# Kernel tuning notes

Measured on AMD Instinct MI355X. Metric: run time of the kernel, lower is better.

The kernel has to match this reference:

```python
import jax, jax.numpy as jnp
import numpy as np

D = 512      # input_dim
A = 512      # inner_att_dim
H = 8        # outer_att_head_n
DK = 64      # outer_att_dim
HS = 4       # outer_score_att_head_n
DKS = 64     # outer_score_att_dim
FF = 2048    # ffn_dim
P = 512      # past_edit_n
E = 256      # number of edit groups
NM = 4       # n_modes
NEG = -999999.0
EPS = 1e-5


def layer_norm(x, w, b):
    mu = x.mean(-1, keepdims=True)
    var = ((x - mu) ** 2).mean(-1, keepdims=True)
    return (x - mu) / jnp.sqrt(var + EPS) * w + b


def setup_inputs() -> dict:
    rng = np.random.default_rng(0)
    lens = rng.integers(128, 385, size=E)
    N = int(lens.sum())
    key = jax.random.key(0)
    ks = jax.random.split(key, 24)

    def w(k, shape, s=0.02):
        return jax.random.normal(k, shape, jnp.float32) * s

    return {
        "x": w(ks[0], (N, D), 1.0),
        "past_rep": w(ks[1], (1, P, D), 1.0),
        "edit_lens": jnp.asarray(lens, jnp.int32),
        "mode": jax.random.randint(ks[2], (N,), 0, NM),
        # inner attention trans1 / trans2
        "t1w1": w(ks[3], (D, A)), "t1b1": jnp.zeros((A,), jnp.float32),
        "t1w2": w(ks[4], (A, D)), "t1b2": jnp.zeros((D,), jnp.float32),
        "t2w1": w(ks[5], (D, A)), "t2b1": jnp.zeros((A,), jnp.float32),
        "t2w2": w(ks[6], (A, 1)), "t2b2": jnp.zeros((1,), jnp.float32),
        # outer attention (with values)
        "oq_w": w(ks[7], (D, H * DK)), "oq_b": jnp.zeros((H * DK,), jnp.float32),
        "ok_w": w(ks[8], (D, H * DK)), "ok_b": jnp.zeros((H * DK,), jnp.float32),
        "ov_w": w(ks[9], (D, H * DK)), "ov_b": jnp.zeros((H * DK,), jnp.float32),
        "oo_w": w(ks[10], (H * DK, D)), "oo_b": jnp.zeros((D,), jnp.float32),
        # outer score attention (scores only)
        "sq_w": w(ks[11], (D, HS * DKS)), "sq_b": jnp.zeros((HS * DKS,), jnp.float32),
        "sk_w": w(ks[12], (D, HS * DKS)), "sk_b": jnp.zeros((HS * DKS,), jnp.float32),
        # feedforward
        "f1w": w(ks[13], (D, FF)), "f1b": jnp.zeros((FF,), jnp.float32),
        "f2w": w(ks[14], (FF, D)), "f2b": jnp.zeros((D,), jnp.float32),
        # layer norms
        "ln1w": jnp.ones((D,), jnp.float32), "ln1b": jnp.zeros((D,), jnp.float32),
        "ln2w": jnp.ones((D,), jnp.float32), "ln2b": jnp.zeros((D,), jnp.float32),
        "ln3w": jnp.ones((D,), jnp.float32), "ln3b": jnp.zeros((D,), jnp.float32),
        # FiLM mode tables (torch init: scale=1, shift=0)
        "mscale": jnp.ones((NM, D), jnp.float32),
        "mshift": jnp.zeros((NM, D), jnp.float32),
    }


def reference(x, past_rep, edit_lens, mode,
              t1w1, t1b1, t1w2, t1b2, t2w1, t2b1, t2w2, t2b2,
              oq_w, oq_b, ok_w, ok_b, ov_w, ov_b, oo_w, oo_b,
              sq_w, sq_b, sk_w, sk_b,
              f1w, f1b, f2w, f2b,
              ln1w, ln1b, ln2w, ln2b, ln3w, ln3b,
              mscale, mshift):
    N = x.shape[0]
    Eg = edit_lens.shape[0]
    Pn = past_rep.shape[1]
    # token -> edit-group id (replaces split/pad/mask gather with segment ops)
    seg = jnp.repeat(jnp.arange(Eg), edit_lens, total_repeat_length=N)

    # ---- inner attention (segment softmax) ----
    att_x = jnp.maximum(x @ t1w1 + t1b1, 0) @ t1w2 + t1b2          # [N, D]
    s = (jnp.maximum(att_x @ t2w1 + t2b1, 0) @ t2w2 + t2b2)[:, 0]  # [N]
    smax = jax.lax.stop_gradient(jax.ops.segment_max(s, seg, num_segments=Eg))
    p = jnp.exp(s - smax[seg])
    den = jax.ops.segment_sum(p, seg, num_segments=Eg)
    wgt = p / den[seg]
    weighted = att_x * wgt[:, None]                                # == masked padded att_x*att_s
    sample_rep = jax.ops.segment_sum(weighted, seg, num_segments=Eg)  # [E, D]
    x = layer_norm(x + weighted, ln1w, ln1b)

    sr = sample_rep[None]                                          # [1, E, D]
    new_rep = jnp.concatenate([past_rep, sr], axis=1)              # [1, P+E, D]
    mask = jnp.triu(jnp.ones((Eg, Pn + Eg), x.dtype), k=Pn + 1) * NEG

    # ---- outer attention (multi-head, with values) ----
    q = (sr @ oq_w + oq_b).reshape(1, Eg, H, DK)
    k = (new_rep @ ok_w + ok_b).reshape(1, Pn + Eg, H, DK)
    v = (new_rep @ ov_w + ov_b).reshape(1, Pn + Eg, H, DK)
    sc = jnp.einsum('bqhd,bkhd->bhqk', q, k) / jnp.sqrt(jnp.asarray(DK, x.dtype)) + mask
    a = jax.nn.softmax(sc, axis=-1)
    o = jnp.einsum('bhqk,bkhd->bqhd', a, v).reshape(1, Eg, H * DK) @ oo_w + oo_b
    x = layer_norm(x + o[0][seg], ln2w, ln2b)                      # repeat_interleave via gather

    # ---- outer score attention (scores only, head-mean) ----
    q2 = (sr @ sq_w + sq_b).reshape(1, Eg, HS, DKS)
    k2 = (new_rep @ sk_w + sk_b).reshape(1, Pn + Eg, HS, DKS)
    sc2 = jnp.einsum('bqhd,bkhd->bhqk', q2, k2) / jnp.sqrt(jnp.asarray(DKS, x.dtype)) + mask
    a2 = jax.nn.softmax(sc2, axis=-1).mean(1)[0]                   # [E, P+E]
    u = jnp.diagonal(a2, offset=Pn)                                # [E]
    pflip = jnp.flip(jnp.cumprod(jnp.flip(1.0 - u)))               # reversed cumprod
    update_scale = jnp.concatenate([u[:-1] * pflip[1:], u[-1:]])
    past_update_scale = pflip[0]

    # ---- FFN + FiLM gate ----
    ffn = jnp.maximum(x @ f1w + f1b, 0) @ f2w + f2b
    x = layer_norm(x + ffn, ln3w, ln3b)
    pre = x * mscale[mode] + mshift[mode]
    x = jnp.maximum(pre, 0) + x
    return (x, past_update_scale, update_scale, new_rep)
```

## Files before the change

kernel.cpp:

```cpp
#include <hip/hip_runtime.h>
#include <hip/hip_bf16.h>
#include <cmath>


#define DD 512
#define FF 2048
#define PP 512
#define NEG_BIG (-1e30f)
#define LDT 68
#define LBUF (128 * 32)

typedef __attribute__((ext_vector_type(8))) short shortx8;
typedef __attribute__((ext_vector_type(4))) float floatx4;

__device__ __forceinline__ unsigned short f2b(float f) {
    unsigned int u = __float_as_uint(f);
    unsigned int r = (u + 0x7fffu + ((u >> 16) & 1u)) >> 16;
    return (unsigned short)r;
}
__device__ __forceinline__ float b2f(unsigned short h) {
    return __uint_as_float(((unsigned int)h) << 16);
}

__device__ __forceinline__ void async_copy16(const void* g, void* l) {
    __builtin_amdgcn_global_load_lds(
        (const __attribute__((address_space(1))) unsigned int*)g,
        (__attribute__((address_space(3))) unsigned int*)l, 16, 0, 0);
}

__device__ __forceinline__ float wave_sum64(float v) {
#pragma unroll
    for (int d = 32; d > 0; d >>= 1) v += __shfl_xor(v, d, 64);
    return v;
}

template<int OUT_BF16, int RELU>
__global__ __launch_bounds__(256) void gemm_bf16_kernel(
    const unsigned short* __restrict__ A, const unsigned short* __restrict__ Bt,
    const float* __restrict__ bias, void* __restrict__ C,
    int M, int N, int K)
{
    __shared__ unsigned short As[3][LBUF];
    __shared__ unsigned short Bs[3][LBUF];

    int t = threadIdx.x;
    int w = t >> 6, l = t & 63;

    int nwg = gridDim.x * gridDim.y;
    int bid = blockIdx.x + blockIdx.y * gridDim.x;
    int qch = nwg >> 3, rch = nwg & 7;
    int xcd = bid & 7, lo = bid >> 3;
    int swz = (xcd < rch ? xcd * (qch + 1) : rch * (qch + 1) + (xcd - rch) * qch) + lo;
    int bm = (swz / gridDim.y) * 128;
    int bn = (swz % gridDim.y) * 128;

    int wm = (w >> 1) * 64, wn = (w & 1) * 64;

    floatx4 acc[4][4];
#pragma unroll
    for (int i = 0; i < 4; ++i)
#pragma unroll
        for (int j = 0; j < 4; ++j)
#pragma unroll
            for (int r = 0; r < 4; ++r) acc[i][j][r] = 0.f;

    int s0 = t, s1 = 256 + t;
    int ar0 = s0 >> 2, ar1 = s1 >> 2;
    int ak0 = ((s0 & 3) ^ ((ar0 >> 1) & 3)) * 8;
    int ak1 = ((s1 & 3) ^ ((ar1 >> 1) & 3)) * 8;
    int am0 = min(bm + ar0, M - 1);
    int am1 = min(bm + ar1, M - 1);
    const unsigned short* Ap0 = A + (size_t)am0 * K + ak0;
    const unsigned short* Ap1 = A + (size_t)am1 * K + ak1;
    const unsigned short* Bp0 = Bt + (size_t)(bn + ar0) * K + ak0;
    const unsigned short* Bp1 = Bt + (size_t)(bn + ar1) * K + ak1;

    int o0 = (w * 64) * 8, o1 = (256 + w * 64) * 8;

    int fr = l & 15, fq = l >> 4;
    int sw = (fr >> 1) & 3;
    int aoff = (wm + fr) * 32 + ((fq ^ sw) * 8);
    int boff = (wn + fr) * 32 + ((fq ^ sw) * 8);

    int nt = K >> 5;

    async_copy16(Ap0, &As[0][o0]);
    async_copy16(Ap1, &As[0][o1]);
    async_copy16(Bp0, &Bs[0][o0]);
    async_copy16(Bp1, &Bs[0][o1]);
    async_copy16(Ap0 + 32, &As[1][o0]);
    async_copy16(Ap1 + 32, &As[1][o1]);
    async_copy16(Bp0 + 32, &Bs[1][o0]);
    async_copy16(Bp1 + 32, &Bs[1][o1]);
    asm volatile("s_waitcnt vmcnt(4)" ::: "memory");
    __builtin_amdgcn_s_barrier();
    asm volatile("" ::: "memory");

    int b0 = 0, b1 = 1, b2 = 2;
    for (int tt = 0; tt < nt; ++tt) {
        if (tt + 2 < nt) {
            int k2 = (tt + 2) << 5;
            unsigned short* Ad = &As[0][0] + b2 * LBUF;
            unsigned short* Bd = &Bs[0][0] + b2 * LBUF;
            async_copy16(Ap0 + k2, Ad + o0);
            async_copy16(Ap1 + k2, Ad + o1);
            async_copy16(Bp0 + k2, Bd + o0);
            async_copy16(Bp1 + k2, Bd + o1);
        }
        {
            const unsigned short* Ab = &As[0][0] + b0 * LBUF;
            const unsigned short* Bb = &Bs[0][0] + b0 * LBUF;
            shortx8 af[4], bf[4];
#pragma unroll
            for (int i = 0; i < 4; ++i) af[i] = *(const shortx8*)&Ab[aoff + i * 16 * 32];
#pragma unroll
            for (int j = 0; j < 4; ++j) bf[j] = *(const shortx8*)&Bb[boff + j * 16 * 32];
#pragma unroll
            for (int i = 0; i < 4; ++i)
#pragma unroll
                for (int j = 0; j < 4; ++j)
                    acc[i][j] = __builtin_amdgcn_mfma_f32_16x16x32_bf16(bf[j], af[i], acc[i][j], 0, 0, 0);
        }
        if (tt + 2 < nt) {
            asm volatile("s_waitcnt vmcnt(4)" ::: "memory");
        } else {
            asm volatile("s_waitcnt vmcnt(0)" ::: "memory");
        }
        __builtin_amdgcn_s_barrier();
        asm volatile("" ::: "memory");
        int tmp = b0; b0 = b1; b1 = b2; b2 = tmp;
    }

    float4 bb[4];
#pragma unroll
    for (int j = 0; j < 4; ++j)
        bb[j] = *(const float4*)&bias[bn + wn + j * 16 + fq * 4];

#pragma unroll
    for (int i = 0; i < 4; ++i) {
        int row = bm + wm + i * 16 + fr;
        if (row >= M) continue;
#pragma unroll
        for (int j = 0; j < 4; ++j) {
            int col = bn + wn + j * 16 + fq * 4;
            float v0 = acc[i][j][0] + bb[j].x;
            float v1 = acc[i][j][1] + bb[j].y;
            float v2 = acc[i][j][2] + bb[j].z;
            float v3 = acc[i][j][3] + bb[j].w;
            if (RELU) {
                v0 = fmaxf(v0, 0.f); v1 = fmaxf(v1, 0.f);
                v2 = fmaxf(v2, 0.f); v3 = fmaxf(v3, 0.f);
            }
            if (OUT_BF16) {
                ushort4 o;
                o.x = f2b(v0); o.y = f2b(v1); o.z = f2b(v2); o.w = f2b(v3);
                *(ushort4*)&((unsigned short*)C)[(size_t)row * N + col] = o;
            } else {
                float4 o;
                o.x = v0; o.y = v1; o.z = v2; o.w = v3;
                *(float4*)&((float*)C)[(size_t)row * N + col] = o;
            }
        }
    }
}

__global__ void cvt_b16_kernel(const float* __restrict__ in, unsigned short* __restrict__ out, size_t n4)
{
    size_t i = (size_t)blockIdx.x * blockDim.x + threadIdx.x;
    if (i >= n4) return;
    float4 v = ((const float4*)in)[i];
    ushort4 o;
    o.x = f2b(v.x); o.y = f2b(v.y); o.z = f2b(v.z); o.w = f2b(v.w);
    ((ushort4*)out)[i] = o;
}

__global__ __launch_bounds__(256) void transpose_b16_kernel(
    const float* __restrict__ W, unsigned short* __restrict__ Wt, int Kd, int Nd)
{
    __shared__ float tile[32][33];
    int bx = blockIdx.x * 32;
    int by = blockIdx.y * 32;
    int tx = threadIdx.x & 31, ty = threadIdx.x >> 5;
#pragma unroll
    for (int i = 0; i < 32; i += 8)
        tile[ty + i][tx] = W[(size_t)(by + ty + i) * Nd + bx + tx];
    __syncthreads();
#pragma unroll
    for (int i = 0; i < 32; i += 8)
        Wt[(size_t)(bx + ty + i) * Kd + by + tx] = f2b(tile[tx][ty + i]);
}

__global__ void bcat_kernel(const float* __restrict__ okb, const float* __restrict__ ovb,
                            const float* __restrict__ oqb, const float* __restrict__ skb,
                            const float* __restrict__ sqb, float* __restrict__ bcat)
{
    int i = blockIdx.x * 256 + threadIdx.x;
    float v;
    if      (i < 512)  v = okb[i];
    else if (i < 1024) v = ovb[i - 512];
    else if (i < 1536) v = oqb[i - 1024];
    else if (i < 1792) v = skb[i - 1536];
    else               v = sqb[i - 1792];
    bcat[i] = v;
}

__global__ __launch_bounds__(256) void gemm_kernel(
    const float* __restrict__ A, const float* __restrict__ W,
    const float* __restrict__ bias, float* __restrict__ C,
    int M, int N, int K, int relu)
{
    __shared__ float As[16][68];
    __shared__ float Ws[16][68];
    int t  = threadIdx.x;
    int tx = t & 15, ty = t >> 4;
    int bm = blockIdx.x * 64, bn = blockIdx.y * 64;
    float acc[4][4] = {};

    for (int k0 = 0; k0 < K; k0 += 16) {
#pragma unroll
        for (int e = 0; e < 4; ++e) {
            int idx = t + e * 256;
            int kk = idx & 15, m = idx >> 4;
            int row = bm + m;
            As[kk][m] = (row < M) ? A[(size_t)row * K + k0 + kk] : 0.f;
        }
#pragma unroll
        for (int e = 0; e < 4; ++e) {
            int idx = t + e * 256;
            int n = idx & 63, kk = idx >> 6;
            Ws[kk][n] = W[(size_t)(k0 + kk) * N + bn + n];
        }
        __syncthreads();
#pragma unroll
        for (int kk = 0; kk < 16; ++kk) {
            float4 a4 = *(const float4*)&As[kk][ty * 4];
            float4 b4 = *(const float4*)&Ws[kk][tx * 4];
            float av[4] = {a4.x, a4.y, a4.z, a4.w};
            float bv[4] = {b4.x, b4.y, b4.z, b4.w};
#pragma unroll
            for (int i = 0; i < 4; ++i)
#pragma unroll
                for (int j = 0; j < 4; ++j)
                    acc[i][j] += av[i] * bv[j];
        }
        __syncthreads();
    }

#pragma unroll
    for (int i = 0; i < 4; ++i) {
        int row = bm + ty * 4 + i;
        if (row >= M) continue;
        int col = bn + tx * 4;
        float4 bb = *(const float4*)&bias[col];
        float4 r;
        r.x = acc[i][0] + bb.x; r.y = acc[i][1] + bb.y;
        r.z = acc[i][2] + bb.z; r.w = acc[i][3] + bb.w;
        if (relu) {
            r.x = fmaxf(r.x, 0.f); r.y = fmaxf(r.y, 0.f);
            r.z = fmaxf(r.z, 0.f); r.w = fmaxf(r.w, 0.f);
        }
        *(float4*)&C[(size_t)row * N + col] = r;
    }
}

__global__ __launch_bounds__(64) void rowdot512_b16_kernel(
    const unsigned short* __restrict__ A, const float* __restrict__ w,
    const float* __restrict__ bptr, float* __restrict__ out)
{
    int row = blockIdx.x;
    int lane = threadIdx.x;
    int col = lane * 8;
    shortx8 a8 = *(const shortx8*)(A + (size_t)row * DD + col);
    float4 w0 = *(const float4*)(w + col);
    float4 w1 = *(const float4*)(w + col + 4);
    float v = b2f((unsigned short)a8[0]) * w0.x + b2f((unsigned short)a8[1]) * w0.y
            + b2f((unsigned short)a8[2]) * w0.z + b2f((unsigned short)a8[3]) * w0.w
            + b2f((unsigned short)a8[4]) * w1.x + b2f((unsigned short)a8[5]) * w1.y
            + b2f((unsigned short)a8[6]) * w1.z + b2f((unsigned short)a8[7]) * w1.w;
#pragma unroll
    for (int d = 32; d > 0; d >>= 1) v += __shfl_down(v, d, 64);
    if (lane == 0) out[row] = v + bptr[0];
}

__global__ void seg_offsets_kernel(const int* __restrict__ lens, int* __restrict__ offs, int E)
{
    if (threadIdx.x == 0 && blockIdx.x == 0) {
        int acc = 0;
        for (int g = 0; g < E; ++g) { offs[g] = acc; acc += lens[g]; }
        offs[E] = acc;
    }
}

__global__ void fill_seg_kernel(const int* __restrict__ offs, int* __restrict__ seg)
{
    int g = blockIdx.x;
    int o = offs[g], e = offs[g + 1];
    for (int i = o + threadIdx.x; i < e; i += blockDim.x) seg[i] = g;
}

__global__ __launch_bounds__(384) void seg_softmax_kernel(
    const float* __restrict__ s, const int* __restrict__ offs, float* __restrict__ wgt)
{
    __shared__ float red[8];
    int g = blockIdx.x;
    int o = offs[g], len = offs[g + 1] - o;
    int t = threadIdx.x;
    int lane = t & 63, wid = t >> 6;

    float v = (t < len) ? s[o + t] : NEG_BIG;
    float m = v;
#pragma unroll
    for (int d = 32; d > 0; d >>= 1) m = fmaxf(m, __shfl_down(m, d, 64));
    if (lane == 0) red[wid] = m;
    __syncthreads();
    if (t == 0) {
        float mm = red[0];
        for (int i = 1; i < 6; ++i) mm = fmaxf(mm, red[i]);
        red[6] = mm;
    }
    __syncthreads();
    float M = red[6];

    float p = (t < len) ? expf(v - M) : 0.f;
    float sum = p;
#pragma unroll
    for (int d = 32; d > 0; d >>= 1) sum += __shfl_down(sum, d, 64);
    if (lane == 0) red[wid] = sum;
    __syncthreads();
    if (t == 0) {
        float ss = red[0];
        for (int i = 1; i < 6; ++i) ss += red[i];
        red[7] = ss;
    }
    __syncthreads();
    if (t < len) wgt[o + t] = p / red[7];
}

__global__ __launch_bounds__(256) void seg_wsum_part_kernel(
    const unsigned short* __restrict__ att_x, const float* __restrict__ wgt,
    const int* __restrict__ offs, float* __restrict__ part)
{
    __shared__ float sm[4][DD];
    int g = blockIdx.x, ch = blockIdx.y;
    int o = offs[g], e = offs[g + 1];
    int len = e - o;
    int per = (len + 7) >> 3;
    int s = o + ch * per;
    int en = min(s + per, e);

    int t = threadIdx.x, lane = t & 63, w = t >> 6;
    int col = lane * 8;
    float acc[8] = {};
    for (int i = s + w; i < en; i += 4) {
        float wt = wgt[i];
        shortx8 v = *(const shortx8*)(att_x + (size_t)i * DD + col);
#pragma unroll
        for (int j = 0; j < 8; ++j)
            acc[j] += b2f((unsigned short)v[j]) * wt;
    }
#pragma unroll
    for (int j = 0; j < 8; ++j) sm[w][col + j] = acc[j];
    __syncthreads();

    float* pr = part + ((size_t)g * 8 + ch) * DD;
#pragma unroll
    for (int j = 0; j < 2; ++j) {
        int c = t * 2 + j;
        pr[c] = (sm[0][c] + sm[1][c]) + (sm[2][c] + sm[3][c]);
    }
}

__global__ __launch_bounds__(256) void seg_wsum_reduce_kernel(
    const float* __restrict__ part, float* __restrict__ rep)
{
    int g = blockIdx.x;
    int t = threadIdx.x;
#pragma unroll
    for (int j = 0; j < 2; ++j) {
        int c = t * 2 + j;
        float s = 0.f;
#pragma unroll
        for (int ch = 0; ch < 8; ++ch)
            s += part[((size_t)g * 8 + ch) * DD + c];
        rep[(size_t)g * DD + c] = s;
    }
}

__global__ __launch_bounds__(256) void ln1_kernel(
    const float* __restrict__ x, const unsigned short* __restrict__ att_x,
    const float* __restrict__ wgt, const float* __restrict__ w,
    const float* __restrict__ b, float* __restrict__ out, int N)
{
    int row = blockIdx.x * 4 + (threadIdx.x >> 6);
    if (row >= N) return;
    int col = (threadIdx.x & 63) * 8;
    const float* xr = x + (size_t)row * DD + col;
    const unsigned short* ar = att_x + (size_t)row * DD + col;
    float wr = wgt[row];
    float4 x0 = *(const float4*)xr;
    float4 x1 = *(const float4*)(xr + 4);
    shortx8 a8 = *(const shortx8*)ar;
    float v[8];
    v[0] = x0.x + b2f((unsigned short)a8[0]) * wr;
    v[1] = x0.y + b2f((unsigned short)a8[1]) * wr;
    v[2] = x0.z + b2f((unsigned short)a8[2]) * wr;
    v[3] = x0.w + b2f((unsigned short)a8[3]) * wr;
    v[4] = x1.x + b2f((unsigned short)a8[4]) * wr;
    v[5] = x1.y + b2f((unsigned short)a8[5]) * wr;
    v[6] = x1.z + b2f((unsigned short)a8[6]) * wr;
    v[7] = x1.w + b2f((unsigned short)a8[7]) * wr;
    float s = (v[0] + v[1] + v[2] + v[3]) + (v[4] + v[5] + v[6] + v[7]);
    float mean = wave_sum64(s) * (1.f / 512.f);
    float q = 0.f;
#pragma unroll
    for (int j = 0; j < 8; ++j) { v[j] -= mean; q += v[j] * v[j]; }
    float rstd = rsqrtf(wave_sum64(q) * (1.f / 512.f) + 1e-5f);
    float4 w0 = *(const float4*)(w + col), w1 = *(const float4*)(w + col + 4);
    float4 b0 = *(const float4*)(b + col), b1 = *(const float4*)(b + col + 4);
    float4 o0, o1;
    o0.x = v[0] * rstd * w0.x + b0.x; o0.y = v[1] * rstd * w0.y + b0.y;
    o0.z = v[2] * rstd * w0.z + b0.z; o0.w = v[3] * rstd * w0.w + b0.w;
    o1.x = v[4] * rstd * w1.x + b1.x; o1.y = v[5] * rstd * w1.y + b1.y;
    o1.z = v[6] * rstd * w1.z + b1.z; o1.w = v[7] * rstd * w1.w + b1.w;
    *(float4*)(out + (size_t)row * DD + col) = o0;
    *(float4*)(out + (size_t)row * DD + col + 4) = o1;
}

__global__ __launch_bounds__(256) void ln2_kernel(
    float* __restrict__ xb, const float* __restrict__ o,
    const int* __restrict__ seg, const float* __restrict__ w,
    const float* __restrict__ b, unsigned short* __restrict__ xb16, int N)
{
    int row = blockIdx.x * 4 + (threadIdx.x >> 6);
    if (row >= N) return;
    int col = (threadIdx.x & 63) * 8;
    int g = seg[row];
    const float* xr = xb + (size_t)row * DD + col;
    const float* orow = o + (size_t)g * DD + col;
    float4 x0 = *(const float4*)xr;
    float4 x1 = *(const float4*)(xr + 4);
    float4 a0 = *(const float4*)orow;
    float4 a1 = *(const float4*)(orow + 4);
    float v[8];
    v[0] = x0.x + a0.x; v[1] = x0.y + a0.y; v[2] = x0.z + a0.z; v[3] = x0.w + a0.w;
    v[4] = x1.x + a1.x; v[5] = x1.y + a1.y; v[6] = x1.z + a1.z; v[7] = x1.w + a1.w;
    float s = (v[0] + v[1] + v[2] + v[3]) + (v[4] + v[5] + v[6] + v[7]);
    float mean = wave_sum64(s) * (1.f / 512.f);
    float q = 0.f;
#pragma unroll
    for (int j = 0; j < 8; ++j) { v[j] -= mean; q += v[j] * v[j]; }
    float rstd = rsqrtf(wave_sum64(q) * (1.f / 512.f) + 1e-5f);
    float4 w0 = *(const float4*)(w + col), w1 = *(const float4*)(w + col + 4);
    float4 b0 = *(const float4*)(b + col), b1 = *(const float4*)(b + col + 4);
    float y[8];
    y[0] = v[0] * rstd * w0.x + b0.x; y[1] = v[1] * rstd * w0.y + b0.y;
    y[2] = v[2] * rstd * w0.z + b0.z; y[3] = v[3] * rstd * w0.w + b0.w;
    y[4] = v[4] * rstd * w1.x + b1.x; y[5] = v[5] * rstd * w1.y + b1.y;
    y[6] = v[6] * rstd * w1.z + b1.z; y[7] = v[7] * rstd * w1.w + b1.w;
    float4 o0, o1;
    o0.x = y[0]; o0.y = y[1]; o0.z = y[2]; o0.w = y[3];
    o1.x = y[4]; o1.y = y[5]; o1.z = y[6]; o1.w = y[7];
    *(float4*)(xb + (size_t)row * DD + col) = o0;
    *(float4*)(xb + (size_t)row * DD + col + 4) = o1;
    ushort4 h0, h1;
    h0.x = f2b(y[0]); h0.y = f2b(y[1]); h0.z = f2b(y[2]); h0.w = f2b(y[3]);
    h1.x = f2b(y[4]); h1.y = f2b(y[5]); h1.z = f2b(y[6]); h1.w = f2b(y[7]);
    *(ushort4*)(xb16 + (size_t)row * DD + col) = h0;
    *(ushort4*)(xb16 + (size_t)row * DD + col + 4) = h1;
}

__global__ __launch_bounds__(256) void ln3_film_kernel(
    const float* __restrict__ xb, const unsigned short* __restrict__ ffn,
    const int* __restrict__ mode, const float* __restrict__ w,
    const float* __restrict__ b, const float* __restrict__ msc,
    const float* __restrict__ msh, float* __restrict__ out, int N)
{
    int row = blockIdx.x * 4 + (threadIdx.x >> 6);
    if (row >= N) return;
    int col = (threadIdx.x & 63) * 8;
    int md = mode[row];
    const float* xr = xb + (size_t)row * DD + col;
    const unsigned short* fr = ffn + (size_t)row * DD + col;
    float4 x0 = *(const float4*)xr;
    float4 x1 = *(const float4*)(xr + 4);
    shortx8 f8 = *(const shortx8*)fr;
    float v[8];
    v[0] = x0.x + b2f((unsigned short)f8[0]);
    v[1] = x0.y + b2f((unsigned short)f8[1]);
    v[2] = x0.z + b2f((unsigned short)f8[2]);
    v[3] = x0.w + b2f((unsigned short)f8[3]);
    v[4] = x1.x + b2f((unsigned short)f8[4]);
    v[5] = x1.y + b2f((unsigned short)f8[5]);
    v[6] = x1.z + b2f((unsigned short)f8[6]);
    v[7] = x1.w + b2f((unsigned short)f8[7]);
    float s = (v[0] + v[1] + v[2] + v[3]) + (v[4] + v[5] + v[6] + v[7]);
    float mean = wave_sum64(s) * (1.f / 512.f);
    float q = 0.f;
#pragma unroll
    for (int j = 0; j < 8; ++j) { v[j] -= mean; q += v[j] * v[j]; }
    float rstd = rsqrtf(wave_sum64(q) * (1.f / 512.f) + 1e-5f);
    float4 w0 = *(const float4*)(w + col), w1 = *(const float4*)(w + col + 4);
    float4 b0 = *(const float4*)(b + col), b1 = *(const float4*)(b + col + 4);
    const float* mscr = msc + (size_t)md * DD + col;
    const float* mshr = msh + (size_t)md * DD + col;
    float4 s0 = *(const float4*)mscr, s1 = *(const float4*)(mscr + 4);
    float4 t0 = *(const float4*)mshr, t1 = *(const float4*)(mshr + 4);
    float y[8], sc[8], sh[8], wv[8], bv[8];
    wv[0] = w0.x; wv[1] = w0.y; wv[2] = w0.z; wv[3] = w0.w;
    wv[4] = w1.x; wv[5] = w1.y; wv[6] = w1.z; wv[7] = w1.w;
    bv[0] = b0.x; bv[1] = b0.y; bv[2] = b0.z; bv[3] = b0.w;
    bv[4] = b1.x; bv[5] = b1.y; bv[6] = b1.z; bv[7] = b1.w;
    sc[0] = s0.x; sc[1] = s0.y; sc[2] = s0.z; sc[3] = s0.w;
    sc[4] = s1.x; sc[5] = s1.y; sc[6] = s1.z; sc[7] = s1.w;
    sh[0] = t0.x; sh[1] = t0.y; sh[2] = t0.z; sh[3] = t0.w;
    sh[4] = t1.x; sh[5] = t1.y; sh[6] = t1.z; sh[7] = t1.w;
    float r[8];
#pragma unroll
    for (int j = 0; j < 8; ++j) {
        y[j] = v[j] * rstd * wv[j] + bv[j];
        float p = y[j] * sc[j] + sh[j];
        r[j] = fmaxf(p, 0.f) + y[j];
    }
    float4 o0, o1;
    o0.x = r[0]; o0.y = r[1]; o0.z = r[2]; o0.w = r[3];
    o1.x = r[4]; o1.y = r[5]; o1.z = r[6]; o1.w = r[7];
    *(float4*)(out + (size_t)row * DD + col) = o0;
    *(float4*)(out + (size_t)row * DD + col + 4) = o1;
}

__global__ void newrep_kernel(const float* __restrict__ past, const float* __restrict__ rep,
                              float* __restrict__ out, int total)
{
    int i = blockIdx.x * blockDim.x + threadIdx.x;
    if (i >= total) return;
    out[i] = (i < PP * DD) ? past[i] : rep[i - PP * DD];
}

__global__ __launch_bounds__(256) void attn_scores_kernel(
    const float* __restrict__ proj, float* __restrict__ S, int pe)
{
    int q0 = blockIdx.x * 64;
    int k0 = blockIdx.y * 64;
    int h  = blockIdx.z;
    if (k0 > PP + q0 + 63) return;

    int qcol = (h < 8) ? (1024 + h * 64) : (1792 + (h - 8) * 64);
    int kcol = (h < 8) ? (h * 64)        : (1536 + (h - 8) * 64);

    __shared__ float Qs[64][LDT];
    __shared__ float Ks[64][LDT];
    int t = threadIdx.x;
    int r = t >> 2, c4 = (t & 3) * 16;
    const float* qsrc = proj + (size_t)(PP + q0 + r) * 2048 + qcol + c4;
    const float* ksrc = proj + (size_t)(k0 + r) * 2048 + kcol + c4;
#pragma unroll
    for (int e = 0; e < 4; ++e) {
        float4 v = *(const float4*)(qsrc + e * 4);
        Qs[c4 + e * 4 + 0][r] = v.x; Qs[c4 + e * 4 + 1][r] = v.y;
        Qs[c4 + e * 4 + 2][r] = v.z; Qs[c4 + e * 4 + 3][r] = v.w;
        float4 u = *(const float4*)(ksrc + e * 4);
        Ks[c4 + e * 4 + 0][r] = u.x; Ks[c4 + e * 4 + 1][r] = u.y;
        Ks[c4 + e * 4 + 2][r] = u.z; Ks[c4 + e * 4 + 3][r] = u.w;
    }
    __syncthreads();

    int tx = t & 15, ty = t >> 4;
    float acc[4][4] = {};
#pragma unroll 4
    for (int d = 0; d < 64; ++d) {
        float4 a = *(const float4*)&Qs[d][ty * 4];
        float4 b = *(const float4*)&Ks[d][tx * 4];
        float av[4] = {a.x, a.y, a.z, a.w};
        float bv[4] = {b.x, b.y, b.z, b.w};
#pragma unroll
        for (int i = 0; i < 4; ++i)
#pragma unroll
            for (int j = 0; j < 4; ++j)
                acc[i][j] += av[i] * bv[j];
    }

    float* Sh = S + ((size_t)h * 256 + q0) * pe + k0;
#pragma unroll
    for (int i = 0; i < 4; ++i) {
        float4 o;
        o.x = acc[i][0] * 0.125f; o.y = acc[i][1] * 0.125f;
        o.z = acc[i][2] * 0.125f; o.w = acc[i][3] * 0.125f;
        *(float4*)&Sh[(size_t)(ty * 4 + i) * pe + tx * 4] = o;
    }
}

__global__ __launch_bounds__(256) void attn_softmax_kernel(
    float* __restrict__ S, float* __restrict__ u4, int pe)
{
    __shared__ float red[8];
    int q = blockIdx.x;
    int h = blockIdx.y;
    int limq = PP + q;
    float* row = S + ((size_t)h * 256 + q) * pe;
    int t = threadIdx.x;
    int lane = t & 63, wid = t >> 6;

    float m = NEG_BIG;
    for (int k = t; k <= limq; k += 256) m = fmaxf(m, row[k]);
#pragma unroll
    for (int d = 32; d > 0; d >>= 1) m = fmaxf(m, __shfl_xor(m, d, 64));
    if (lane == 0) red[wid] = m;
    __syncthreads();
    float M = fmaxf(fmaxf(red[0], red[1]), fmaxf(red[2], red[3]));

    float s = 0.f;
    for (int k = t; k <= limq; k += 256) s += expf(row[k] - M);
#pragma unroll
    for (int d = 32; d > 0; d >>= 1) s += __shfl_xor(s, d, 64);
    if (lane == 0) red[4 + wid] = s;
    __syncthreads();
    float SUM = (red[4] + red[5]) + (red[6] + red[7]);
    float inv = 1.f / SUM;

    if (h < 8) {
        for (int k = t; k < pe; k += 256)
            row[k] = (k <= limq) ? expf(row[k] - M) * inv : 0.f;
    } else {
        if (t == 0) u4[q * 4 + (h - 8)] = expf(row[limq] - M) * inv;
    }
}

__global__ __launch_bounds__(256) void attn_pv_kernel(
    const float* __restrict__ S, const float* __restrict__ proj,
    float* __restrict__ ob, int pe)
{
    __shared__ float Ps[64][36];
    __shared__ float Vs[64][LDT];
    int q0 = blockIdx.x * 32;
    int h  = blockIdx.y;
    int ktiles = (PP + q0 + 31) / 64 + 1;

    int t = threadIdx.x;
    int tx = t & 15, ty = t >> 4;
    int rp = t >> 3, c8 = (t & 7) * 8;
    int rv = t >> 2, c16 = (t & 3) * 16;
    float acc[2][4] = {};

    for (int kt = 0; kt < ktiles; ++kt) {
        int k0 = kt * 64;
        const float* psrc = S + ((size_t)h * 256 + q0 + rp) * pe + k0 + c8;
        const float* vsrc = proj + (size_t)(k0 + rv) * 2048 + 512 + h * 64 + c16;
#pragma unroll
        for (int e = 0; e < 2; ++e) {
            float4 v = *(const float4*)(psrc + e * 4);
            Ps[c8 + e * 4 + 0][rp] = v.x; Ps[c8 + e * 4 + 1][rp] = v.y;
            Ps[c8 + e * 4 + 2][rp] = v.z; Ps[c8 + e * 4 + 3][rp] = v.w;
        }
#pragma unroll
        for (int e = 0; e < 4; ++e)
            *(float4*)&Vs[rv][c16 + e * 4] = *(const float4*)(vsrc + e * 4);
        __syncthreads();

#pragma unroll 8
        for (int kk = 0; kk < 64; ++kk) {
            float2 a = *(const float2*)&Ps[kk][ty * 2];
            float4 b = *(const float4*)&Vs[kk][tx * 4];
            float av[2] = {a.x, a.y};
            float bv[4] = {b.x, b.y, b.z, b.w};
#pragma unroll
            for (int i = 0; i < 2; ++i)
#pragma unroll
                for (int j = 0; j < 4; ++j)
                    acc[i][j] += av[i] * bv[j];
        }
        __syncthreads();
    }

#pragma unroll
    for (int i = 0; i < 2; ++i) {
        float4 o;
        o.x = acc[i][0]; o.y = acc[i][1]; o.z = acc[i][2]; o.w = acc[i][3];
        *(float4*)&ob[(size_t)(q0 + ty * 2 + i) * DD + h * 64 + tx * 4] = o;
    }
}

__global__ void finalize_kernel(const float* __restrict__ u4, float* __restrict__ out_past,
                                float* __restrict__ out_us, int E)
{
    if (threadIdx.x == 0 && blockIdx.x == 0) {
        float uE = 0.25f * (u4[(E - 1) * 4] + u4[(E - 1) * 4 + 1] + u4[(E - 1) * 4 + 2] + u4[(E - 1) * 4 + 3]);
        out_us[E - 1] = uE;
        float pf = 1.f;
        for (int i = E - 1; i >= 0; --i) {
            float u = 0.25f * (u4[i * 4] + u4[i * 4 + 1] + u4[i * 4 + 2] + u4[i * 4 + 3]);
            if (i < E - 1) out_us[i] = u * pf;
            pf = (1.f - u) * pf;
        }
        out_past[0] = pf;
    }
}

extern "C" void kernel_launch(void* const* d_in, const int* in_sizes, int n_in,
                              void* d_out, int out_size, void* d_ws, size_t ws_size,
                              hipStream_t stream)
{
    const float* x    = (const float*)d_in[0];
    const float* past = (const float*)d_in[1];
    const int*   lens = (const int*)d_in[2];
    const int*   mode = (const int*)d_in[3];
    const float* t1w1 = (const float*)d_in[4];
    const float* t1b1 = (const float*)d_in[5];
    const float* t1w2 = (const float*)d_in[6];
    const float* t1b2 = (const float*)d_in[7];
    const float* t2w1 = (const float*)d_in[8];
    const float* t2b1 = (const float*)d_in[9];
    const float* t2w2 = (const float*)d_in[10];
    const float* t2b2 = (const float*)d_in[11];
    const float* oq_w = (const float*)d_in[12];
    const float* oq_b = (const float*)d_in[13];
    const float* ok_w = (const float*)d_in[14];
    const float* ok_b = (const float*)d_in[15];
    const float* ov_w = (const float*)d_in[16];
    const float* ov_b = (const float*)d_in[17];
    const float* oo_w = (const float*)d_in[18];
    const float* oo_b = (const float*)d_in[19];
    const float* sq_w = (const float*)d_in[20];
    const float* sq_b = (const float*)d_in[21];
    const float* sk_w = (const float*)d_in[22];
    const float* sk_b = (const float*)d_in[23];
    const float* f1w  = (const float*)d_in[24];
    const float* f1b  = (const float*)d_in[25];
    const float* f2w  = (const float*)d_in[26];
    const float* f2b_ = (const float*)d_in[27];
    const float* ln1w = (const float*)d_in[28];
    const float* ln1b = (const float*)d_in[29];
    const float* ln2w = (const float*)d_in[30];
    const float* ln2b = (const float*)d_in[31];
    const float* ln3w = (const float*)d_in[32];
    const float* ln3b = (const float*)d_in[33];
    const float* msc  = (const float*)d_in[34];
    const float* msh  = (const float*)d_in[35];

    int N  = in_sizes[0] / DD;
    int E  = in_sizes[2];
    int PE = PP + E;
    if (N <= 0) return;

    float* out        = (float*)d_out;
    float* out_x      = out;
    float* out_past   = out + (size_t)N * DD;
    float* out_us     = out_past + 1;
    float* out_newrep = out_us + E;

    const int CH = 16384;
    char* wp = (char*)d_ws;
    unsigned short* b16_a = (unsigned short*)wp;  wp += (size_t)N * DD * 2;
    unsigned short* b16_b = (unsigned short*)wp;  wp += (size_t)N * DD * 2;
    unsigned short* ffh   = (unsigned short*)wp;  wp += (size_t)CH * FF * 2;
    unsigned short* wt1   = (unsigned short*)wp;  wp += (size_t)DD * DD * 2;
    unsigned short* wt2   = (unsigned short*)wp;  wp += (size_t)DD * DD * 2;
    unsigned short* wt3   = (unsigned short*)wp;  wp += (size_t)DD * DD * 2;
    unsigned short* wtf1  = (unsigned short*)wp;  wp += (size_t)FF * DD * 2;
    unsigned short* wtf2  = (unsigned short*)wp;  wp += (size_t)DD * FF * 2;
    unsigned short* wtcat = (unsigned short*)wp;  wp += (size_t)2048 * DD * 2;
    unsigned short* nr16  = (unsigned short*)wp;  wp += (size_t)PE * DD * 2;
    float* bcat = (float*)wp;  wp += 2048 * 4;
    float* proj = (float*)wp;  wp += (size_t)PE * 2048 * 4;
    float* sbuf = (float*)wp;  wp += (size_t)N * 4;
    float* wgt  = (float*)wp;  wp += (size_t)N * 4;
    float* rep  = (float*)wp;  wp += (size_t)E * DD * 4;
    float* ob   = (float*)wp;  wp += (size_t)E * DD * 4;
    float* oprj = (float*)wp;  wp += (size_t)E * DD * 4;
    float* u4   = (float*)wp;  wp += (size_t)E * 4 * 4;
    int*   seg  = (int*)wp;    wp += (size_t)N * 4;
    int*   offs = (int*)wp;

    float* part = (float*)ffh;
    float* S    = (float*)ffh;

    int mg128 = (N + 127) / 128;
    int ln_grid = (N + 3) / 4;

    transpose_b16_kernel<<<dim3(DD / 32, DD / 32), 256, 0, stream>>>(t1w1, wt1, DD, DD);
    transpose_b16_kernel<<<dim3(DD / 32, DD / 32), 256, 0, stream>>>(t1w2, wt2, DD, DD);
    transpose_b16_kernel<<<dim3(DD / 32, DD / 32), 256, 0, stream>>>(t2w1, wt3, DD, DD);
    transpose_b16_kernel<<<dim3(FF / 32, DD / 32), 256, 0, stream>>>(f1w, wtf1, DD, FF);
    transpose_b16_kernel<<<dim3(DD / 32, FF / 32), 256, 0, stream>>>(f2w, wtf2, FF, DD);
    transpose_b16_kernel<<<dim3(DD / 32, DD / 32), 256, 0, stream>>>(ok_w, wtcat,              DD, DD);
    transpose_b16_kernel<<<dim3(DD / 32, DD / 32), 256, 0, stream>>>(ov_w, wtcat + 512 * DD,  DD, DD);
    transpose_b16_kernel<<<dim3(DD / 32, DD / 32), 256, 0, stream>>>(oq_w, wtcat + 1024 * DD, DD, DD);
    transpose_b16_kernel<<<dim3(256 / 32, DD / 32), 256, 0, stream>>>(sk_w, wtcat + 1536 * DD, DD, 256);
    transpose_b16_kernel<<<dim3(256 / 32, DD / 32), 256, 0, stream>>>(sq_w, wtcat + 1792 * DD, DD, 256);
    bcat_kernel<<<8, 256, 0, stream>>>(ok_b, ov_b, oq_b, sk_b, sq_b, bcat);

    size_t n4 = (size_t)N * DD / 4;
    cvt_b16_kernel<<<(int)((n4 + 255) / 256), 256, 0, stream>>>(x, b16_a, n4);

    gemm_bf16_kernel<1, 1><<<dim3(mg128, DD / 128), 256, 0, stream>>>(b16_a, wt1, t1b1, b16_b, N, DD, DD);
    gemm_bf16_kernel<1, 0><<<dim3(mg128, DD / 128), 256, 0, stream>>>(b16_b, wt2, t1b2, b16_a, N, DD, DD);
    gemm_bf16_kernel<1, 1><<<dim3(mg128, DD / 128), 256, 0, stream>>>(b16_a, wt3, t2b1, b16_b, N, DD, DD);
    rowdot512_b16_kernel<<<N, 64, 0, stream>>>(b16_b, t2w2, t2b2, sbuf);

    seg_offsets_kernel<<<1, 64, 0, stream>>>(lens, offs, E);
    fill_seg_kernel<<<E, 256, 0, stream>>>(offs, seg);
    seg_softmax_kernel<<<E, 384, 0, stream>>>(sbuf, offs, wgt);
    seg_wsum_part_kernel<<<dim3(E, 8), 256, 0, stream>>>(b16_a, wgt, offs, part);
    seg_wsum_reduce_kernel<<<E, 256, 0, stream>>>(part, rep);
    ln1_kernel<<<ln_grid, 256, 0, stream>>>(x, b16_a, wgt, ln1w, ln1b, out_x, N);

    int nr_total = PE * DD;
    newrep_kernel<<<(nr_total + 255) / 256, 256, 0, stream>>>(past, rep, out_newrep, nr_total);
    cvt_b16_kernel<<<(nr_total / 4 + 255) / 256, 256, 0, stream>>>(out_newrep, nr16, nr_total / 4);

    gemm_bf16_kernel<0, 0><<<dim3(PE / 128, 2048 / 128), 256, 0, stream>>>(nr16, wtcat, bcat, proj, PE, 2048, DD);

    attn_scores_kernel<<<dim3(E / 64, PE / 64, 12), 256, 0, stream>>>(proj, S, PE);
    attn_softmax_kernel<<<dim3(E, 12), 256, 0, stream>>>(S, u4, PE);
    attn_pv_kernel<<<dim3(E / 32, 8), 256, 0, stream>>>(S, proj, ob, PE);
    gemm_kernel<<<dim3(E / 64, DD / 64), 256, 0, stream>>>(ob, oo_w, oo_b, oprj, E, DD, DD, 0);
    ln2_kernel<<<ln_grid, 256, 0, stream>>>(out_x, oprj, seg, ln2w, ln2b, b16_b, N);
    finalize_kernel<<<1, 64, 0, stream>>>(u4, out_past, out_us, E);

    for (int r0 = 0; r0 < N; r0 += CH) {
        int mr = N - r0; if (mr > CH) mr = CH;
        int mgc = (mr + 127) / 128;
        gemm_bf16_kernel<1, 1><<<dim3(mgc, FF / 128), 256, 0, stream>>>(
            b16_b + (size_t)r0 * DD, wtf1, f1b, ffh, mr, FF, DD);
        gemm_bf16_kernel<1, 0><<<dim3(mgc, DD / 128), 256, 0, stream>>>(
            ffh, wtf2, f2b_, b16_a + (size_t)r0 * DD, mr, DD, FF);
    }
    ln3_film_kernel<<<ln_grid, 256, 0, stream>>>(out_x, b16_a, mode, ln3w, ln3b, msc, msh, out_x, N);
}
```

Baseline: 1.412 ms.

## Process two M-tiles per workgroup in bf16 GEMM and enlarge FFN chunk size

Adds a STRIP template parameter so each workgroup computes two consecutive 128-row tiles sharing one continuous pipelined K loop, writing back and resetting accumulators between tiles. The wrapper picks STRIP=2 only when the halved grid still has at least 512 workgroups, cutting workgroup count and launch/prologue overhead. The FFN chunk size now covers all rows when the workspace is large enough, giving fewer, larger GEMM launches. Risks: B tiles are reloaded per strip rather than reused, and fewer workgroups can reduce occupancy balance.

```diff
diff --git a/kernel.cpp b/kernel.cpp
--- a/kernel.cpp
+++ b/kernel.cpp
@@ -34,7 +34,7 @@
     return v;
 }
 
-template<int OUT_BF16, int RELU>
+template<int OUT_BF16, int RELU, int STRIP>
 __global__ __launch_bounds__(256) void gemm_bf16_kernel(
     const unsigned short* __restrict__ A, const unsigned short* __restrict__ Bt,
     const float* __restrict__ bias, void* __restrict__ C,
@@ -51,8 +51,8 @@
     int qch = nwg >> 3, rch = nwg & 7;
     int xcd = bid & 7, lo = bid >> 3;
     int swz = (xcd < rch ? xcd * (qch + 1) : rch * (qch + 1) + (xcd - rch) * qch) + lo;
-    int bm = (swz / gridDim.y) * 128;
-    int bn = (swz % gridDim.y) * 128;
+    int bmb = (swz / gridDim.y) * (128 * STRIP);
+    int bn  = (swz % gridDim.y) * 128;
 
     int wm = (w >> 1) * 64, wn = (w & 1) * 64;
 
@@ -68,10 +68,15 @@
     int ar0 = s0 >> 2, ar1 = s1 >> 2;
     int ak0 = ((s0 & 3) ^ ((ar0 >> 1) & 3)) * 8;
     int ak1 = ((s1 & 3) ^ ((ar1 >> 1) & 3)) * 8;
-    int am0 = min(bm + ar0, M - 1);
-    int am1 = min(bm + ar1, M - 1);
-    const unsigned short* Ap0 = A + (size_t)am0 * K + ak0;
-    const unsigned short* Ap1 = A + (size_t)am1 * K + ak1;
+
+    const unsigned short* Ap0m0 = A + (size_t)min(bmb + ar0, M - 1) * K + ak0;
+    const unsigned short* Ap1m0 = A + (size_t)min(bmb + ar1, M - 1) * K + ak1;
+    const unsigned short* Ap0m1 = Ap0m0;
+    const unsigned short* Ap1m1 = Ap1m0;
+    if (STRIP == 2) {
+        Ap0m1 = A + (size_t)min(bmb + 128 + ar0, M - 1) * K + ak0;
+        Ap1m1 = A + (size_t)min(bmb + 128 + ar1, M - 1) * K + ak1;
+    }
     const unsigned short* Bp0 = Bt + (size_t)(bn + ar0) * K + ak0;
     const unsigned short* Bp1 = Bt + (size_t)(bn + ar1) * K + ak1;
 
@@ -83,29 +88,41 @@
     int boff = (wn + fr) * 32 + ((fq ^ sw) * 8);
 
     int nt = K >> 5;
-
-    async_copy16(Ap0, &As[0][o0]);
-    async_copy16(Ap1, &As[0][o1]);
+    int T  = nt * STRIP;
+
+    async_copy16(Ap0m0, &As[0][o0]);
+    async_copy16(Ap1m0, &As[0][o1]);
     async_copy16(Bp0, &Bs[0][o0]);
     async_copy16(Bp1, &Bs[0][o1]);
-    async_copy16(Ap0 + 32, &As[1][o0]);
-    async_copy16(Ap1 + 32, &As[1][o1]);
+    async_copy16(Ap0m0 + 32, &As[1][o0]);
+    async_copy16(Ap1m0 + 32, &As[1][o1]);
     async_copy16(Bp0 + 32, &Bs[1][o0]);
     async_copy16(Bp1 + 32, &Bs[1][o1]);
     asm volatile("s_waitcnt vmcnt(4)" ::: "memory");
     __builtin_amdgcn_s_barrier();
     asm volatile("" ::: "memory");
 
+    float4 bb[4];
+#pragma unroll
+    for (int j = 0; j < 4; ++j)
+        bb[j] = *(const float4*)&bias[bn + wn + j * 16 + fq * 4];
+
     int b0 = 0, b1 = 1, b2 = 2;
-    for (int tt = 0; tt < nt; ++tt) {
-        if (tt + 2 < nt) {
-            int k2 = (tt + 2) << 5;
+    int ck = 0, cm = 0;
+    for (int tau = 0; tau < T; ++tau) {
+        if (tau + 2 < T) {
+            int t2 = tau + 2;
+            int usem1 = (STRIP == 2 && t2 >= nt) ? 1 : 0;
+            int k2 = t2 - (usem1 ? nt : 0);
+            int kb = k2 << 5;
+            const unsigned short* a0p = usem1 ? Ap0m1 : Ap0m0;
+            const unsigned short* a1p = usem1 ? Ap1m1 : Ap1m0;
             unsigned short* Ad = &As[0][0] + b2 * LBUF;
             unsigned short* Bd = &Bs[0][0] + b2 * LBUF;
-            async_copy16(Ap0 + k2, Ad + o0);
-            async_copy16(Ap1 + k2, Ad + o1);
-            async_copy16(Bp0 + k2, Bd + o0);
-            async_copy16(Bp1 + k2, Bd + o1);
+            async_copy16(a0p + kb, Ad + o0);
+            async_copy16(a1p + kb, Ad + o1);
+            async_copy16(Bp0 + kb, Bd + o0);
+            async_copy16(Bp1 + kb, Bd + o1);
         }
         {
             const unsigned short* Ab = &As[0][0] + b0 * LBUF;
@@ -121,7 +138,7 @@
                 for (int j = 0; j < 4; ++j)
                     acc[i][j] = __builtin_amdgcn_mfma_f32_16x16x32_bf16(bf[j], af[i], acc[i][j], 0, 0, 0);
         }
-        if (tt + 2 < nt) {
+        if (tau + 2 < T) {
             asm volatile("s_waitcnt vmcnt(4)" ::: "memory");
         } else {
             asm volatile("s_waitcnt vmcnt(0)" ::: "memory");
@@ -129,37 +146,46 @@
         __builtin_amdgcn_s_barrier();
         asm volatile("" ::: "memory");
         int tmp = b0; b0 = b1; b1 = b2; b2 = tmp;
-    }
-
-    float4 bb[4];
-#pragma unroll
-    for (int j = 0; j < 4; ++j)
-        bb[j] = *(const float4*)&bias[bn + wn + j * 16 + fq * 4];
-
-#pragma unroll
-    for (int i = 0; i < 4; ++i) {
-        int row = bm + wm + i * 16 + fr;
-        if (row >= M) continue;
-#pragma unroll
-        for (int j = 0; j < 4; ++j) {
-            int col = bn + wn + j * 16 + fq * 4;
-            float v0 = acc[i][j][0] + bb[j].x;
-            float v1 = acc[i][j][1] + bb[j].y;
-            float v2 = acc[i][j][2] + bb[j].z;
-            float v3 = acc[i][j][3] + bb[j].w;
-            if (RELU) {
-                v0 = fmaxf(v0, 0.f); v1 = fmaxf(v1, 0.f);
-                v2 = fmaxf(v2, 0.f); v3 = fmaxf(v3, 0.f);
+
+        if (++ck == nt) {
+            ck = 0;
+            int rb = bmb + cm * 128 + wm;
+#pragma unroll
+            for (int i = 0; i < 4; ++i) {
+                int row = rb + i * 16 + fr;
+                if (row < M) {
+#pragma unroll
+                    for (int j = 0; j < 4; ++j) {
+                        int col = bn + wn + j * 16 + fq * 4;
+                        float v0 = acc[i][j][0] + bb[j].x;
+                        float v1 = acc[i][j][1] + bb[j].y;
+                        float v2 = acc[i][j][2] + bb[j].z;
+                        float v3 = acc[i][j][3] + bb[j].w;
+                        if (RELU) {
+                            v0 = fmaxf(v0, 0.f); v1 = fmaxf(v1, 0.f);
+                            v2 = fmaxf(v2, 0.f); v3 = fmaxf(v3, 0.f);
+                        }
+                        if (OUT_BF16) {
+                            ushort4 o;
+                            o.x = f2b(v0); o.y = f2b(v1); o.z = f2b(v2); o.w = f2b(v3);
+                            *(ushort4*)&((unsigned short*)C)[(size_t)row * N + col] = o;
+                        } else {
+                            float4 o;
+                            o.x = v0; o.y = v1; o.z = v2; o.w = v3;
+                            *(float4*)&((float*)C)[(size_t)row * N + col] = o;
+                        }
+                    }
+                }
             }
-            if (OUT_BF16) {
-                ushort4 o;
-                o.x = f2b(v0); o.y = f2b(v1); o.z = f2b(v2); o.w = f2b(v3);
-                *(ushort4*)&((unsigned short*)C)[(size_t)row * N + col] = o;
-            } else {
-                float4 o;
-                o.x = v0; o.y = v1; o.z = v2; o.w = v3;
-                *(float4*)&((float*)C)[(size_t)row * N + col] = o;
+            if (STRIP == 2 && cm + 1 < STRIP) {
+#pragma unroll
+                for (int i = 0; i < 4; ++i)
+#pragma unroll
+                    for (int j = 0; j < 4; ++j)
+#pragma unroll
+                        for (int r = 0; r < 4; ++r) acc[i][j][r] = 0.f;
             }
+            ++cm;
         }
     }
 }
@@ -692,6 +718,21 @@
             pf = (1.f - u) * pf;
         }
         out_past[0] = pf;
+    }
+}
+
+template<int OB, int RL>
+static void run_gemm(const unsigned short* A, const unsigned short* Bt,
+                     const float* bias, void* C, int M, int Nc, int K,
+                     hipStream_t st)
+{
+    int mg = (M + 127) / 128;
+    int ntile = Nc / 128;
+    int gx2 = (mg + 1) / 2;
+    if (mg >= 2 && gx2 * ntile >= 512) {
+        gemm_bf16_kernel<OB, RL, 2><<<dim3(gx2, ntile), 256, 0, st>>>(A, Bt, bias, C, M, Nc, K);
+    } else {
+        gemm_bf16_kernel<OB, RL, 1><<<dim3(mg, ntile), 256, 0, st>>>(A, Bt, bias, C, M, Nc, K);
     }
 }
 
@@ -747,7 +788,21 @@
     float* out_us     = out_past + 1;
     float* out_newrep = out_us + E;
 
-    const int CH = 16384;
+    size_t CHf = ((size_t)N + 127) / 128 * 128;
+    size_t fixed = (size_t)N * DD * 2 * 2
+                 + 3 * (size_t)DD * DD * 2
+                 + (size_t)FF * DD * 2 + (size_t)DD * FF * 2
+                 + (size_t)2048 * DD * 2
+                 + (size_t)PE * DD * 2
+                 + 2048 * 4
+                 + (size_t)PE * 2048 * 4
+                 + (size_t)N * 4 * 2
+                 + (size_t)E * DD * 4 * 3
+                 + (size_t)E * 16
+                 + (size_t)N * 4
+                 + (size_t)(E + 1) * 4 + 1024;
+    int CH = (fixed + CHf * (size_t)FF * 2 <= ws_size) ? (int)CHf : 16384;
+
     char* wp = (char*)d_ws;
     unsigned short* b16_a = (unsigned short*)wp;  wp += (size_t)N * DD * 2;
     unsigned short* b16_b = (unsigned short*)wp;  wp += (size_t)N * DD * 2;
@@ -773,7 +828,6 @@
     float* part = (float*)ffh;
     float* S    = (float*)ffh;
 
-    int mg128 = (N + 127) / 128;
     int ln_grid = (N + 3) / 4;
 
     transpose_b16_kernel<<<dim3(DD / 32, DD / 32), 256, 0, stream>>>(t1w1, wt1, DD, DD);
@@ -791,9 +845,9 @@
     size_t n4 = (size_t)N * DD / 4;
     cvt_b16_kernel<<<(int)((n4 + 255) / 256), 256, 0, stream>>>(x, b16_a, n4);
 
-    gemm_bf16_kernel<1, 1><<<dim3(mg128, DD / 128), 256, 0, stream>>>(b16_a, wt1, t1b1, b16_b, N, DD, DD);
-    gemm_bf16_kernel<1, 0><<<dim3(mg128, DD / 128), 256, 0, stream>>>(b16_b, wt2, t1b2, b16_a, N, DD, DD);
-    gemm_bf16_kernel<1, 1><<<dim3(mg128, DD / 128), 256, 0, stream>>>(b16_a, wt3, t2b1, b16_b, N, DD, DD);
+    run_gemm<1, 1>(b16_a, wt1, t1b1, b16_b, N, DD, DD, stream);
+    run_gemm<1, 0>(b16_b, wt2, t1b2, b16_a, N, DD, DD, stream);
+    run_gemm<1, 1>(b16_a, wt3, t2b1, b16_b, N, DD, DD, stream);
     rowdot512_b16_kernel<<<N, 64, 0, stream>>>(b16_b, t2w2, t2b2, sbuf);
 
     seg_offsets_kernel<<<1, 64, 0, stream>>>(lens, offs, E);
@@ -807,7 +861,7 @@
     newrep_kernel<<<(nr_total + 255) / 256, 256, 0, stream>>>(past, rep, out_newrep, nr_total);
     cvt_b16_kernel<<<(nr_total / 4 + 255) / 256, 256, 0, stream>>>(out_newrep, nr16, nr_total / 4);
 
-    gemm_bf16_kernel<0, 0><<<dim3(PE / 128, 2048 / 128), 256, 0, stream>>>(nr16, wtcat, bcat, proj, PE, 2048, DD);
+    run_gemm<0, 0>(nr16, wtcat, bcat, proj, PE, 2048, DD, stream);
 
     attn_scores_kernel<<<dim3(E / 64, PE / 64, 12), 256, 0, stream>>>(proj, S, PE);
     attn_softmax_kernel<<<dim3(E, 12), 256, 0, stream>>>(S, u4, PE);
@@ -818,11 +872,8 @@
 
     for (int r0 = 0; r0 < N; r0 += CH) {
         int mr = N - r0; if (mr > CH) mr = CH;
-        int mgc = (mr + 127) / 128;
-        gemm_bf16_kernel<1, 1><<<dim3(mgc, FF / 128), 256, 0, stream>>>(
-            b16_b + (size_t)r0 * DD, wtf1, f1b, ffh, mr, FF, DD);
-        gemm_bf16_kernel<1, 0><<<dim3(mgc, DD / 128), 256, 0, stream>>>(
-            ffh, wtf2, f2b_, b16_a + (size_t)r0 * DD, mr, DD, FF);
+        run_gemm<1, 1>(b16_b + (size_t)r0 * DD, wtf1, f1b, ffh, mr, FF, DD, stream);
+        run_gemm<1, 0>(ffh, wtf2, f2b_, b16_a + (size_t)r0 * DD, mr, DD, FF, stream);
     }
     ln3_film_kernel<<<ln_grid, 256, 0, stream>>>(out_x, b16_a, mode, ln3w, ln3b, msc, msh, out_x, N);
 }
```

Result: slower. 1.811 ms (+28.3%).
